# Performance work log

Hardware: AMD Instinct MI355X
Metric: run time of the kernel (lower is better)

The kernel has to match this reference:

```python
import jax, jax.numpy as jnp
import numpy as np
import math

N, E, H, A = 50000, 800000, 128, 8
D = H // A


def setup_inputs() -> dict:
    key = jax.random.key(0)
    ks = jax.random.split(key, 12)
    q = jax.random.normal(ks[0], (N, H), dtype=jnp.float32)
    k = jax.random.normal(ks[1], (N, H), dtype=jnp.float32)
    v = jax.random.normal(ks[2], (N, H), dtype=jnp.float32)
    Wq = jax.random.normal(ks[3], (H, H), dtype=jnp.float32) * 0.05
    bq = jax.random.normal(ks[4], (H,), dtype=jnp.float32) * 0.05
    Wk = jax.random.normal(ks[5], (H, H), dtype=jnp.float32) * 0.05
    bk = jax.random.normal(ks[6], (H,), dtype=jnp.float32) * 0.05
    Wv = jax.random.normal(ks[7], (H, H), dtype=jnp.float32) * 0.05
    bv = jax.random.normal(ks[8], (H,), dtype=jnp.float32) * 0.05
    # Ensure every node id appears at least once in q_indices so that
    # q_indices.unique() == arange(N) and the output shape is static [N, H].
    tail = jax.random.randint(ks[9], (E - N,), 0, N)
    q_indices = jnp.concatenate([jnp.arange(N), tail]).astype(jnp.int32)
    k_indices = jax.random.randint(ks[10], (E,), 0, N).astype(jnp.int32)
    return {"q": q, "k": k, "v": v, "Wq": Wq, "bq": bq, "Wk": Wk, "bk": bk,
            "Wv": Wv, "bv": bv, "q_indices": q_indices, "k_indices": k_indices}


def reference(q, k, v, Wq, bq, Wk, bk, Wv, bv, q_indices, k_indices):
    n = q.shape[0]
    # Gather node features per edge (irregular access).
    qe = q[q_indices]            # [E, H]
    ke = k[k_indices]            # [E, H]
    ve = v[k_indices]            # [E, H]
    # Linear projections (torch Linear: x @ W.T + b), split heads -> [E, A, D].
    Q = (qe @ Wq.T + bq).reshape(-1, A, D)
    K = (ke @ Wk.T + bk).reshape(-1, A, D)
    V = (ve @ Wv.T + bv).reshape(-1, A, D)
    # Per-edge scaled dot-product scores: [E, A].
    scores = jnp.einsum('ead,ead->ea', Q, K) / math.sqrt(D)
    # Segment softmax over edges sharing the same destination node
    # (faithful to the original: plain exp, no max subtraction).
    ex = jnp.exp(scores)                                        # [E, A]
    denom = jax.ops.segment_sum(ex, q_indices, num_segments=n)  # [N, A]
    probs = ex / denom[q_indices]                               # [E, A]
    # Scatter-aggregate weighted values per destination node: [N, A, D].
    ctx = jax.ops.segment_sum(probs[:, :, None] * V, q_indices, num_segments=n)
    # Merge heads -> [N, H].
    return ctx.reshape(n, A * D)
```

## Files before the change

kernel.cpp:

```cpp
#include <hip/hip_runtime.h>
#include <hip/hip_bf16.h>

#define HDIM 128
#define LDS_STRIDE 136

typedef __attribute__((ext_vector_type(8))) short bf16x8;
typedef __attribute__((ext_vector_type(4))) float f32x4;

__device__ inline unsigned short f2bf(float f) {
    return __builtin_bit_cast(unsigned short, __float2bfloat16(f));
}
__device__ inline float bflo(unsigned u) { return __uint_as_float(u << 16); }
__device__ inline float bfhi(unsigned u) { return __uint_as_float(u & 0xffff0000u); }

__global__ void init_kernel(int* __restrict__ deg, int n,
                            const float* __restrict__ Wq, const float* __restrict__ Wk,
                            const float* __restrict__ Wv, unsigned short* __restrict__ Wopt) {
    int i = blockIdx.x * 256 + threadIdx.x;
    if (i < n) deg[i] = 0;
    if (i < 3 * HDIM * HDIM) {
        int j  = i & 7;
        int l  = (i >> 3) & 63;
        int ks = (i >> 9) & 3;
        int nt = (i >> 11) & 7;
        int m  = i >> 14;
        const float* W = (m == 0) ? Wq : (m == 1) ? Wk : Wv;
        int row = nt * 16 + (l & 15);
        int col = ks * 32 + ((l >> 4) << 3) + j;
        Wopt[i] = f2bf(W[row * HDIM + col]);
    }
}

__global__ void proj_deg(const float* __restrict__ qin, const float* __restrict__ kin,
                         const float* __restrict__ vin, const unsigned short* __restrict__ Wopt,
                         const float* __restrict__ bq, const float* __restrict__ bk,
                         const float* __restrict__ bv,
                         unsigned short* __restrict__ Qb, unsigned short* __restrict__ KVb,
                         const int* __restrict__ qidx, int* __restrict__ deg,
                         int* __restrict__ rank, int E, int n, int nbx, int ndeg, int ntot)
{
    __shared__ unsigned short tile[64 * LDS_STRIDE];

    const int id     = blockIdx.x;
    const int before = (int)(((long)id * ndeg) / ntot);
    const bool isdeg = (int)(((long)(id + 1) * ndeg) / ntot) > before;

    if (isdeg) {
        const int e0 = before * 1024 + (int)threadIdx.x * 4;
        if (e0 + 4 <= E) {
            const int4 qi = *(const int4*)&qidx[e0];
            int4 r;
            r.x = atomicAdd(&deg[qi.x], 1);
            r.y = atomicAdd(&deg[qi.y], 1);
            r.z = atomicAdd(&deg[qi.z], 1);
            r.w = atomicAdd(&deg[qi.w], 1);
            *(int4*)&rank[e0] = r;
        } else {
            #pragma unroll
            for (int j = 0; j < 4; ++j)
                if (e0 + j < E) rank[e0 + j] = atomicAdd(&deg[qidx[e0 + j]], 1);
        }
        return;
    }

    const int pid = id - before;
    const int m   = pid / nbx;
    const int bx  = pid - m * nbx;

    const int tid  = threadIdx.x;
    const int lane = tid & 63;
    const int wv   = tid >> 6;
    const long node0 = (long)bx * 64;

    const float* x = (m == 0) ? qin : (m == 1) ? kin : vin;
    const float* b = (m == 0) ? bq  : (m == 1) ? bk  : bv;
    const unsigned short* Wm = Wopt + (size_t)m * HDIM * HDIM;

    #pragma unroll
    for (int it = 0; it < 8; ++it) {
        int f   = it * 256 + tid;
        int row = f >> 5;
        int c4  = f & 31;
        long node = node0 + row;
        float4 val = make_float4(0.f, 0.f, 0.f, 0.f);
        if (node < n) val = ((const float4*)(x + node * HDIM))[c4];
        ushort4 h;
        h.x = f2bf(val.x); h.y = f2bf(val.y); h.z = f2bf(val.z); h.w = f2bf(val.w);
        *(ushort4*)&tile[row * LDS_STRIDE + c4 * 4] = h;
    }
    __syncthreads();

    const int r15  = lane & 15;
    const int quad = lane >> 4;

    bf16x8 af[4];
    #pragma unroll
    for (int ks = 0; ks < 4; ++ks)
        af[ks] = *(const bf16x8*)&tile[(wv * 16 + r15) * LDS_STRIDE + quad * 8 + ks * 32];

    f32x4 acc[8];
    #pragma unroll
    for (int nt = 0; nt < 8; ++nt) {
        acc[nt] = (f32x4){0.f, 0.f, 0.f, 0.f};
        #pragma unroll
        for (int ks = 0; ks < 4; ++ks) {
            const bf16x8 wfrag =
                *(const bf16x8*)(Wm + ((size_t)((nt * 4 + ks) * 64) + lane) * 8);
            acc[nt] = __builtin_amdgcn_mfma_f32_16x16x32_bf16(af[ks], wfrag, acc[nt], 0, 0, 0);
        }
    }
    __syncthreads();

    #pragma unroll
    for (int nt = 0; nt < 8; ++nt) {
        const int c = nt * 16 + r15;
        const float bias = b[c];
        #pragma unroll
        for (int r = 0; r < 4; ++r)
            tile[(wv * 16 + quad * 4 + r) * LDS_STRIDE + c] = f2bf(acc[nt][r] + bias);
    }
    __syncthreads();

    #pragma unroll
    for (int it = 0; it < 4; ++it) {
        int g   = it * 256 + tid;
        int row = g >> 4;
        int col = (g & 15) * 8;
        long node = node0 + row;
        if (node < n) {
            ushort4 lo = *(const ushort4*)&tile[row * LDS_STRIDE + col];
            ushort4 hi = *(const ushort4*)&tile[row * LDS_STRIDE + col + 4];
            uint2 plo, phi;
            plo.x = (unsigned)lo.x | ((unsigned)lo.y << 16);
            plo.y = (unsigned)lo.z | ((unsigned)lo.w << 16);
            phi.x = (unsigned)hi.x | ((unsigned)hi.y << 16);
            phi.y = (unsigned)hi.z | ((unsigned)hi.w << 16);
            if (m == 0) {
                uint4 out4; out4.x = plo.x; out4.y = plo.y; out4.z = phi.x; out4.w = phi.y;
                *(uint4*)&Qb[node * HDIM + col] = out4;
            } else {
                size_t base = (size_t)node * 256 + (size_t)col * 2 + ((m == 2) ? 4 : 0);
                *(uint2*)&KVb[base]     = plo;
                *(uint2*)&KVb[base + 8] = phi;
            }
        }
    }
}

__global__ void scan_block(const int* __restrict__ deg, int* __restrict__ offs,
                           int* __restrict__ bsum, int n) {
    __shared__ int ws[17];
    const int tid = threadIdx.x;
    const int lane = tid & 63, wv = tid >> 6;
    int i = blockIdx.x * 1024 + tid;
    int v = (i < n) ? deg[i] : 0;
    int sc = v;
    #pragma unroll
    for (int d = 1; d < 64; d <<= 1) {
        int t = __shfl_up(sc, d, 64);
        if (lane >= d) sc += t;
    }
    if (lane == 63) ws[wv] = sc;
    __syncthreads();
    if (tid == 0) {
        int base = 0;
        #pragma unroll
        for (int w = 0; w < 16; ++w) { int t = ws[w]; ws[w] = base; base += t; }
        ws[16] = base;
    }
    __syncthreads();
    if (i < n) offs[i] = ws[wv] + (sc - v);
    if (tid == 0) bsum[blockIdx.x] = ws[16];
}

__global__ void scan_addtops(const int* __restrict__ bsum, int* __restrict__ offs,
                             int n, int E, int nb) {
    __shared__ int s_base;
    const int tid = threadIdx.x;
    if (tid < 64) {
        int v = (tid < nb) ? bsum[tid] : 0;
        int sc = v;
        #pragma unroll
        for (int d = 1; d < 64; d <<= 1) {
            int t = __shfl_up(sc, d, 64);
            if (tid >= d) sc += t;
        }
        if (tid == blockIdx.x) s_base = sc - v;
    }
    __syncthreads();
    int i = blockIdx.x * 1024 + tid;
    if (i < n) offs[i] += s_base;
    if (blockIdx.x == 0 && tid == 0) offs[n] = E;
}

__global__ void fill_kernel(const int* __restrict__ qidx, const int* __restrict__ kidx,
                            const int* __restrict__ offs, const int* __restrict__ rank,
                            int* __restrict__ srcl, int E) {
    int e0 = (blockIdx.x * 256 + (int)threadIdx.x) * 4;
    if (e0 + 4 <= E) {
        const int4 qi = *(const int4*)&qidx[e0];
        const int4 ki = *(const int4*)&kidx[e0];
        const int4 rk = *(const int4*)&rank[e0];
        srcl[offs[qi.x] + rk.x] = ki.x;
        srcl[offs[qi.y] + rk.y] = ki.y;
        srcl[offs[qi.z] + rk.z] = ki.z;
        srcl[offs[qi.w] + rk.w] = ki.w;
    } else {
        #pragma unroll
        for (int j = 0; j < 4; ++j)
            if (e0 + j < E) srcl[offs[qidx[e0 + j]] + rank[e0 + j]] = kidx[e0 + j];
    }
}

__global__ void agg_kernel(const uint2* __restrict__ Q2, const uint4* __restrict__ KV4,
                           const int* __restrict__ offs, const int* __restrict__ srcl,
                           float* __restrict__ out, int n)
{
    const int tid  = threadIdx.x;
    const int l32  = tid & 31;
    const int node = blockIdx.x * 8 + (tid >> 5);
    if (node >= n) return;

    const uint2 qp = Q2[(size_t)node * 32 + l32];
    const float qx = bflo(qp.x), qy = bfhi(qp.x), qz = bflo(qp.y), qw = bfhi(qp.y);

    float dsum = 0.f, a0 = 0.f, a1 = 0.f, a2 = 0.f, a3 = 0.f;
    const int beg = offs[node], end = offs[node + 1];
    const int srcbase = tid & 32;

#define EDGE_STEP(kv)                                                          \
    {                                                                          \
        float part = qx * bflo((kv).x) + qy * bfhi((kv).x)                     \
                   + qz * bflo((kv).y) + qw * bfhi((kv).y);                    \
        part += __shfl_xor(part, 1, 64);                                       \
        part += __shfl_xor(part, 2, 64);                                       \
        float w = __expf(part * 0.25f);                                        \
        dsum += w;                                                             \
        a0 += w * bflo((kv).z); a1 += w * bfhi((kv).z);                        \
        a2 += w * bflo((kv).w); a3 += w * bfhi((kv).w);                        \
    }

    for (int base = beg; base < end; base += 32) {
        int cnt = min(32, end - base);
        int my = (base + l32 < end) ? srcl[base + l32] : 0;
        int j = 0;
        for (; j + 4 <= cnt; j += 4) {
            int s0 = __shfl(my, srcbase + j,     64);
            int s1 = __shfl(my, srcbase + j + 1, 64);
            int s2 = __shfl(my, srcbase + j + 2, 64);
            int s3 = __shfl(my, srcbase + j + 3, 64);
            uint4 kv0 = KV4[(size_t)s0 * 32 + l32];
            uint4 kv1 = KV4[(size_t)s1 * 32 + l32];
            uint4 kv2 = KV4[(size_t)s2 * 32 + l32];
            uint4 kv3 = KV4[(size_t)s3 * 32 + l32];
            EDGE_STEP(kv0); EDGE_STEP(kv1); EDGE_STEP(kv2); EDGE_STEP(kv3);
        }
        for (; j < cnt; ++j) {
            int s = __shfl(my, srcbase + j, 64);
            uint4 kv = KV4[(size_t)s * 32 + l32];
            EDGE_STEP(kv);
        }
    }
#undef EDGE_STEP

    float inv = 1.f / dsum;
    float4 r = make_float4(a0 * inv, a1 * inv, a2 * inv, a3 * inv);
    *(float4*)&out[(size_t)node * HDIM + l32 * 4] = r;
}

extern "C" void kernel_launch(void* const* d_in, const int* in_sizes, int n_in,
                              void* d_out, int out_size, void* d_ws, size_t ws_size,
                              hipStream_t stream) {
    const float* q  = (const float*)d_in[0];
    const float* k  = (const float*)d_in[1];
    const float* v  = (const float*)d_in[2];
    const float* Wq = (const float*)d_in[3];
    const float* bq = (const float*)d_in[4];
    const float* Wk = (const float*)d_in[5];
    const float* bk = (const float*)d_in[6];
    const float* Wv = (const float*)d_in[7];
    const float* bv = (const float*)d_in[8];
    const int* qidx = (const int*)d_in[9];
    const int* kidx = (const int*)d_in[10];
    float* out = (float*)d_out;

    const int N = in_sizes[0] / HDIM;
    const int E = in_sizes[9];

    char* p = (char*)d_ws;
    unsigned short* Qb  = (unsigned short*)p; p += (size_t)N * HDIM * sizeof(unsigned short);
    unsigned short* KVb = (unsigned short*)p; p += (size_t)2 * N * HDIM * sizeof(unsigned short);
    unsigned short* Wopt = (unsigned short*)p; p += (size_t)3 * HDIM * HDIM * sizeof(unsigned short);
    int* deg  = (int*)p; p += (size_t)N * sizeof(int);
    int* offs = (int*)p; p += (size_t)(N + 1) * sizeof(int);
    int* bsum = (int*)p; p += 64 * sizeof(int);
    int* rank = (int*)p; p += (size_t)E * sizeof(int);
    int* srcl = (int*)p; p += (size_t)E * sizeof(int);

    const int nbx  = (N + 63) / 64;
    const int ndeg = (E + 1023) / 1024;
    const int ntot = 3 * nbx + ndeg;
    const int nfb  = (E + 1023) / 1024;
    const int nb   = (N + 1023) / 1024;
    const int initn = (N > 3 * HDIM * HDIM) ? N : 3 * HDIM * HDIM;

    init_kernel<<<(initn + 255) / 256, 256, 0, stream>>>(deg, N, Wq, Wk, Wv, Wopt);
    proj_deg<<<ntot, 256, 0, stream>>>(q, k, v, Wopt, bq, bk, bv, Qb, KVb,
                                       qidx, deg, rank, E, N, nbx, ndeg, ntot);
    scan_block<<<nb, 1024, 0, stream>>>(deg, offs, bsum, N);
    scan_addtops<<<nb, 1024, 0, stream>>>(bsum, offs, N, E, nb);
    fill_kernel<<<nfb, 256, 0, stream>>>(qidx, kidx, offs, rank, srcl, E);
    agg_kernel<<<(N + 7) / 8, 256, 0, stream>>>((const uint2*)Qb, (const uint4*)KVb,
                                                offs, srcl, out, N);
}
```

Measured before the change: 245.6 us.

## Fuse K and V projections per block and load MFMA fragments directly from global

The projection kernel now has each block handle either Q or both K and V for its 64 nodes, so the grid shrinks from three projection groups to two. The K and V outputs are interleaved in a per-wave LDS tile and written to KVb as full 16-byte stores instead of split 8-byte stores. A-fragments are read straight from global memory into registers and converted to bf16, removing the shared input staging and all block-level barriers. The cost is fewer, longer-running blocks with more register pressure and less coalesced input loads.

```diff
diff --git a/kernel.cpp b/kernel.cpp
--- a/kernel.cpp
+++ b/kernel.cpp
@@ -2,7 +2,7 @@
 #include <hip/hip_bf16.h>
 
 #define HDIM 128
-#define LDS_STRIDE 136
+#define OSTR 264
 
 typedef __attribute__((ext_vector_type(8))) short bf16x8;
 typedef __attribute__((ext_vector_type(4))) float f32x4;
@@ -12,6 +12,15 @@
 }
 __device__ inline float bflo(unsigned u) { return __uint_as_float(u << 16); }
 __device__ inline float bfhi(unsigned u) { return __uint_as_float(u & 0xffff0000u); }
+
+__device__ inline bf16x8 pack8(float4 a, float4 b) {
+    bf16x8 r;
+    r[0] = (short)f2bf(a.x); r[1] = (short)f2bf(a.y);
+    r[2] = (short)f2bf(a.z); r[3] = (short)f2bf(a.w);
+    r[4] = (short)f2bf(b.x); r[5] = (short)f2bf(b.y);
+    r[6] = (short)f2bf(b.z); r[7] = (short)f2bf(b.w);
+    return r;
+}
 
 __global__ void init_kernel(int* __restrict__ deg, int n,
                             const float* __restrict__ Wq, const float* __restrict__ Wk,
@@ -39,7 +48,7 @@
                          const int* __restrict__ qidx, int* __restrict__ deg,
                          int* __restrict__ rank, int E, int n, int nbx, int ndeg, int ntot)
 {
-    __shared__ unsigned short tile[64 * LDS_STRIDE];
+    __shared__ unsigned short tile[4][16 * OSTR];
 
     const int id     = blockIdx.x;
     const int before = (int)(((long)id * ndeg) / ntot);
@@ -64,87 +73,116 @@
     }
 
     const int pid = id - before;
-    const int m   = pid / nbx;
-    const int bx  = pid - m * nbx;
+    const bool isQ = (pid < nbx);
+    const int bx  = isQ ? pid : (pid - nbx);
 
     const int tid  = threadIdx.x;
     const int lane = tid & 63;
     const int wv   = tid >> 6;
-    const long node0 = (long)bx * 64;
-
-    const float* x = (m == 0) ? qin : (m == 1) ? kin : vin;
-    const float* b = (m == 0) ? bq  : (m == 1) ? bk  : bv;
-    const unsigned short* Wm = Wopt + (size_t)m * HDIM * HDIM;
-
-    #pragma unroll
-    for (int it = 0; it < 8; ++it) {
-        int f   = it * 256 + tid;
-        int row = f >> 5;
-        int c4  = f & 31;
-        long node = node0 + row;
-        float4 val = make_float4(0.f, 0.f, 0.f, 0.f);
-        if (node < n) val = ((const float4*)(x + node * HDIM))[c4];
-        ushort4 h;
-        h.x = f2bf(val.x); h.y = f2bf(val.y); h.z = f2bf(val.z); h.w = f2bf(val.w);
-        *(ushort4*)&tile[row * LDS_STRIDE + c4 * 4] = h;
-    }
-    __syncthreads();
-
     const int r15  = lane & 15;
     const int quad = lane >> 4;
+    const long node0 = (long)bx * 64;
+    const long nodeA = node0 + wv * 16 + r15;
+    unsigned short* lq = tile[wv];
+
+#define LOAD_AF(src)                                                           \
+    {                                                                          \
+        if (nodeA < n) {                                                       \
+            const float* xr = (src) + nodeA * HDIM + quad * 8;                 \
+            _Pragma("unroll")                                                  \
+            for (int ks = 0; ks < 4; ++ks) {                                   \
+                float4 lo = *(const float4*)(xr + ks * 32);                    \
+                float4 hi = *(const float4*)(xr + ks * 32 + 4);                \
+                af[ks] = pack8(lo, hi);                                        \
+            }                                                                  \
+        } else {                                                               \
+            _Pragma("unroll")                                                  \
+            for (int ks = 0; ks < 4; ++ks)                                     \
+                af[ks] = (bf16x8){0, 0, 0, 0, 0, 0, 0, 0};                     \
+        }                                                                      \
+    }
+
+#define MFMA_ALL(Wm)                                                           \
+    {                                                                          \
+        _Pragma("unroll")                                                      \
+        for (int nt = 0; nt < 8; ++nt) {                                       \
+            acc[nt] = (f32x4){0.f, 0.f, 0.f, 0.f};                             \
+            _Pragma("unroll")                                                  \
+            for (int ks = 0; ks < 4; ++ks) {                                   \
+                const bf16x8 wfrag =                                           \
+                    *(const bf16x8*)((Wm) + ((size_t)((nt * 4 + ks) * 64) + lane) * 8); \
+                acc[nt] = __builtin_amdgcn_mfma_f32_16x16x32_bf16(af[ks], wfrag, acc[nt], 0, 0, 0); \
+            }                                                                  \
+        }                                                                      \
+    }
 
     bf16x8 af[4];
-    #pragma unroll
-    for (int ks = 0; ks < 4; ++ks)
-        af[ks] = *(const bf16x8*)&tile[(wv * 16 + r15) * LDS_STRIDE + quad * 8 + ks * 32];
-
-    f32x4 acc[8];
-    #pragma unroll
-    for (int nt = 0; nt < 8; ++nt) {
-        acc[nt] = (f32x4){0.f, 0.f, 0.f, 0.f};
-        #pragma unroll
-        for (int ks = 0; ks < 4; ++ks) {
-            const bf16x8 wfrag =
-                *(const bf16x8*)(Wm + ((size_t)((nt * 4 + ks) * 64) + lane) * 8);
-            acc[nt] = __builtin_amdgcn_mfma_f32_16x16x32_bf16(af[ks], wfrag, acc[nt], 0, 0, 0);
-        }
-    }
-    __syncthreads();
-
-    #pragma unroll
-    for (int nt = 0; nt < 8; ++nt) {
-        const int c = nt * 16 + r15;
-        const float bias = b[c];
-        #pragma unroll
-        for (int r = 0; r < 4; ++r)
-            tile[(wv * 16 + quad * 4 + r) * LDS_STRIDE + c] = f2bf(acc[nt][r] + bias);
-    }
-    __syncthreads();
-
-    #pragma unroll
-    for (int it = 0; it < 4; ++it) {
-        int g   = it * 256 + tid;
-        int row = g >> 4;
-        int col = (g & 15) * 8;
-        long node = node0 + row;
-        if (node < n) {
-            ushort4 lo = *(const ushort4*)&tile[row * LDS_STRIDE + col];
-            ushort4 hi = *(const ushort4*)&tile[row * LDS_STRIDE + col + 4];
-            uint2 plo, phi;
-            plo.x = (unsigned)lo.x | ((unsigned)lo.y << 16);
-            plo.y = (unsigned)lo.z | ((unsigned)lo.w << 16);
-            phi.x = (unsigned)hi.x | ((unsigned)hi.y << 16);
-            phi.y = (unsigned)hi.z | ((unsigned)hi.w << 16);
-            if (m == 0) {
-                uint4 out4; out4.x = plo.x; out4.y = plo.y; out4.z = phi.x; out4.w = phi.y;
-                *(uint4*)&Qb[node * HDIM + col] = out4;
-            } else {
-                size_t base = (size_t)node * 256 + (size_t)col * 2 + ((m == 2) ? 4 : 0);
-                *(uint2*)&KVb[base]     = plo;
-                *(uint2*)&KVb[base + 8] = phi;
+    f32x4  acc[8];
+
+    if (isQ) {
+        LOAD_AF(qin);
+        MFMA_ALL(Wopt);
+        #pragma unroll
+        for (int nt = 0; nt < 8; ++nt) {
+            const int c = nt * 16 + r15;
+            const float bias = bq[c];
+            #pragma unroll
+            for (int r = 0; r < 4; ++r)
+                lq[(quad * 4 + r) * OSTR + c] = f2bf(acc[nt][r] + bias);
+        }
+        #pragma unroll
+        for (int it = 0; it < 4; ++it) {
+            int g   = it * 64 + lane;
+            int row = g >> 4;
+            int col = (g & 15) * 8;
+            long node = node0 + wv * 16 + row;
+            if (node < n) {
+                ushort4 lo = *(const ushort4*)&lq[row * OSTR + col];
+                ushort4 hi = *(const ushort4*)&lq[row * OSTR + col + 4];
+                uint4 o;
+                o.x = (unsigned)lo.x | ((unsigned)lo.y << 16);
+                o.y = (unsigned)lo.z | ((unsigned)lo.w << 16);
+                o.z = (unsigned)hi.x | ((unsigned)hi.y << 16);
+                o.w = (unsigned)hi.z | ((unsigned)hi.w << 16);
+                *(uint4*)&Qb[node * HDIM + col] = o;
             }
         }
-    }
+    } else {
+        LOAD_AF(kin);
+        MFMA_ALL(Wopt + HDIM * HDIM);
+        #pragma unroll
+        for (int nt = 0; nt < 8; ++nt) {
+            const int c = nt * 16 + r15;
+            const float bias = bk[c];
+            const int  slot = (c >> 2) * 8 + (c & 3);
+            #pragma unroll
+            for (int r = 0; r < 4; ++r)
+                lq[(quad * 4 + r) * OSTR + slot] = f2bf(acc[nt][r] + bias);
+        }
+        LOAD_AF(vin);
+        MFMA_ALL(Wopt + 2 * HDIM * HDIM);
+        #pragma unroll
+        for (int nt = 0; nt < 8; ++nt) {
+            const int c = nt * 16 + r15;
+            const float bias = bv[c];
+            const int  slot = (c >> 2) * 8 + 4 + (c & 3);
+            #pragma unroll
+            for (int r = 0; r < 4; ++r)
+                lq[(quad * 4 + r) * OSTR + slot] = f2bf(acc[nt][r] + bias);
+        }
+        #pragma unroll
+        for (int it = 0; it < 8; ++it) {
+            int g   = it * 64 + lane;
+            int row = g >> 5;
+            int ch  = g & 31;
+            long node = node0 + wv * 16 + row;
+            if (node < n)
+                *(uint4*)&KVb[(size_t)node * 256 + ch * 8] =
+                    *(const uint4*)&lq[row * OSTR + ch * 8];
+        }
+    }
+#undef LOAD_AF
+#undef MFMA_ALL
 }
 
 __global__ void scan_block(const int* __restrict__ deg, int* __restrict__ offs,
@@ -299,7 +337,7 @@
 
     const int nbx  = (N + 63) / 64;
     const int ndeg = (E + 1023) / 1024;
-    const int ntot = 3 * nbx + ndeg;
+    const int ntot = 2 * nbx + ndeg;
     const int nfb  = (E + 1023) / 1024;
     const int nb   = (N + 1023) / 1024;
     const int initn = (N > 3 * HDIM * HDIM) ? N : 3 * HDIM * HDIM;
```

Measured after the change: 240.8 us. No clear change (-2.0%).
